# Performance work log

Measured on AMD Instinct MI355X. Metric: run time of the kernel, lower is better.

The kernel has to match this reference:

```python
import jax, jax.numpy as jnp
import numpy as np

IN_FEATURE = 256
OUT_FEATURE = 128
ALPHA = 0.5  # LeakyReLU negative slope
NEG_BIG = -9e15


def setup_inputs() -> dict:
    key = jax.random.key(0)
    k1, k2, k3, k4 = jax.random.split(key, 4)
    N = 8192
    x = jax.random.normal(k1, (N, IN_FEATURE), dtype=jnp.float32)
    adj = jax.random.randint(k2, (N, N), 0, 2, dtype=jnp.int32)
    stdv = 1.0 / np.sqrt(OUT_FEATURE)
    W = jax.random.uniform(k3, (IN_FEATURE, OUT_FEATURE), dtype=jnp.float32,
                           minval=-stdv, maxval=stdv)
    a = jax.random.uniform(k4, (2 * OUT_FEATURE, 1), dtype=jnp.float32,
                           minval=-stdv, maxval=stdv)
    return {"input": x, "adj": adj, "W": W, "a": a}


def reference(input, adj, W, a):
    # h: [N, F_out]
    h = input @ W
    # Additive attention: cat([h_i, h_j]) @ a == h_i @ a1 + h_j @ a2
    a1 = a[:OUT_FEATURE, 0]   # [F_out]
    a2 = a[OUT_FEATURE:, 0]   # [F_out]
    f1 = h @ a1               # [N]  (row / source contribution)
    f2 = h @ a2               # [N]  (col / target contribution)
    e = jax.nn.leaky_relu(f1[:, None] + f2[None, :], negative_slope=ALPHA)  # [N, N]
    scores = jnp.where(adj > 0, e, NEG_BIG)
    attention = jax.nn.softmax(scores, axis=1)  # [N, N]
    h_prime = attention @ h                     # [N, F_out]
    return jax.nn.elu(h_prime)
```

## Files before the change

kernel.cpp:

```cpp
#include <hip/hip_runtime.h>

#define N_NODES 8192
#define IN_F 256
#define OUT_F 128
#define ALPHA 0.5f
#define JC 8
#define KCHUNK 1024
#define ROUNDS 4
#define RSTEPS 8

using short8 = __attribute__((ext_vector_type(8))) short;
using f32x4  = __attribute__((ext_vector_type(4))) float;

__device__ __forceinline__ unsigned short f2bf(float f){
  unsigned int u = __float_as_uint(f);
  u += 0x7fffu + ((u >> 16) & 1u);
  return (unsigned short)(u >> 16);
}

__global__ __launch_bounds__(256) void k_h(const float* __restrict__ x,
                                           const float* __restrict__ W,
                                           float* __restrict__ h){
  __shared__ float xs[16*IN_F];
  const int tid = threadIdx.x;
  const int r0 = blockIdx.x * 16;
  const float4* xg = (const float4*)(x + (size_t)r0*IN_F);
  float4* xl = (float4*)xs;
  #pragma unroll
  for(int i=0;i<4;i++) xl[tid + i*256] = xg[tid + i*256];
  __syncthreads();
  const int wave = tid >> 6, lane = tid & 63;
  float2 acc[4];
  #pragma unroll
  for(int j=0;j<4;j++){ acc[j].x = 0.f; acc[j].y = 0.f; }
  const float2* Wp = (const float2*)W;
  for(int k4=0;k4<IN_F;k4+=4){
    float4 xq[4];
    #pragma unroll
    for(int j=0;j<4;j++) xq[j] = *(const float4*)&xs[(wave*4+j)*IN_F + k4];
    #pragma unroll
    for(int kk=0;kk<4;kk++){
      float2 wv = Wp[(size_t)(k4+kk)*64 + lane];
      #pragma unroll
      for(int j=0;j<4;j++){
        float xv = kk==0?xq[j].x : kk==1?xq[j].y : kk==2?xq[j].z : xq[j].w;
        acc[j].x += xv*wv.x; acc[j].y += xv*wv.y;
      }
    }
  }
  #pragma unroll
  for(int j=0;j<4;j++)
    *(float2*)(h + (size_t)(r0 + wave*4 + j)*OUT_F + lane*2) = acc[j];
}

__global__ __launch_bounds__(256) void k_f(const float* __restrict__ h,
                                           const float* __restrict__ a,
                                           float* __restrict__ f1,
                                           float* __restrict__ f2){
  const int wave = threadIdx.x >> 6, lane = threadIdx.x & 63;
  const int row = blockIdx.x*4 + wave;
  float2 hv = ((const float2*)(h + (size_t)row*OUT_F))[lane];
  float2 a1 = ((const float2*)a)[lane];
  float2 a2 = ((const float2*)(a + OUT_F))[lane];
  float s1 = hv.x*a1.x + hv.y*a1.y;
  float s2 = hv.x*a2.x + hv.y*a2.y;
  #pragma unroll
  for(int off=32; off; off>>=1){
    s1 += __shfl_down(s1, off);
    s2 += __shfl_down(s2, off);
  }
  if(lane == 0){ f1[row] = s1; f2[row] = s2; }
}

#define LDW 132
__global__ __launch_bounds__(256) void k_pack(const float* __restrict__ h,
                                              unsigned short* __restrict__ P){
  __shared__ float ld[32*LDW];
  const int tid = threadIdx.x;
  const int kb = blockIdx.x, j0 = kb*32;
  #pragma unroll
  for(int i=0;i<4;i++){
    int idx = tid + i*256;
    int row = idx >> 5, c4 = (idx & 31)*4;
    *(float4*)&ld[row*LDW + c4] = *(const float4*)(h + (size_t)(j0+row)*OUT_F + c4);
  }
  __syncthreads();
  #pragma unroll
  for(int i=0;i<2;i++){
    int o = tid*2 + i;
    int c = o >> 6, lane = o & 63;
    int q = lane >> 4, n = lane & 15;
    short8 v;
    #pragma unroll
    for(int t=0;t<8;t++) v[t] = (short)f2bf(ld[(q*8+t)*LDW + c*16 + n]);
    *(short8*)(P + ((size_t)(kb*8 + c)*64 + lane)*8) = v;
  }
}

__global__ __launch_bounds__(256, 2) void k_attn(const int* __restrict__ adj,
    const unsigned short* __restrict__ P,
    const float* __restrict__ f1, const float* __restrict__ f2,
    float* __restrict__ part, float* __restrict__ denp){
  __shared__ __align__(16) short Blds[32768];
  const int tid = threadIdx.x;
  const int wave = tid >> 6, lane = tid & 63;
  const int m = lane & 15, q = lane >> 4;
  const int jc = blockIdx.x;
  const int rb = blockIdx.y;
  const int r0w = rb*128 + wave*32;
  const int kb0 = jc * (KCHUNK/32);
  const float rf1a = f1[r0w + m];
  const float rf1b = f1[r0w + 16 + m];
  const int* ap0 = adj + (size_t)(r0w + m)*N_NODES + jc*KCHUNK + q*8;
  const int* ap1 = ap0 + (size_t)16*N_NODES;
  const float* f2p = f2 + jc*KCHUNK + q*8;
  const short8* Pv = (const short8*)P;

  f32x4 acc0[8], acc1[8];
  #pragma unroll
  for(int c=0;c<8;c++){ acc0[c] = (f32x4){0,0,0,0}; acc1[c] = (f32x4){0,0,0,0}; }
  float den0 = 0.f, den1 = 0.f;

  int4 A00 = *(const int4*)(ap0);
  int4 A01 = *(const int4*)(ap0 + 4);
  int4 A10 = *(const int4*)(ap1);
  int4 A11 = *(const int4*)(ap1 + 4);

  auto welem8 = [&](const int4& a, const int4& b, const float4& fa,
                    const float4& fb, float rf1, float& den) -> short8 {
    short8 af; float tv, ev, w;
    #define WE(slot, av, fv)                               \
      tv = rf1 + (fv);                                     \
      ev = tv > 0.f ? tv : ALPHA*tv;                       \
      w  = __expf(ev);                                     \
      w  = ((av) > 0) ? w : 0.f;                           \
      den += w;                                            \
      af[slot] = (short)f2bf(w);
    WE(0,a.x,fa.x) WE(1,a.y,fa.y) WE(2,a.z,fa.z) WE(3,a.w,fa.w)
    WE(4,b.x,fb.x) WE(5,b.y,fb.y) WE(6,b.z,fb.z) WE(7,b.w,fb.w)
    #undef WE
    return af;
  };

  for(int rd=0; rd<ROUNDS; rd++){
    const short8* Ps = Pv + (size_t)(kb0 + rd*8) * 512;
    short8* Bl8 = (short8*)Blds;
    #pragma unroll
    for(int i=0;i<16;i++){
      int idx = i*256 + tid;
      Bl8[idx] = Ps[idx];
    }
    __syncthreads();
    for(int s=0; s<RSTEPS; s++){
      const int gs = rd*RSTEPS + s;
      int4 B00=A00, B01=A01, B10=A10, B11=A11;
      if(gs+1 < ROUNDS*RSTEPS){
        B00 = *(const int4*)(ap0 + (gs+1)*32);
        B01 = *(const int4*)(ap0 + (gs+1)*32 + 4);
        B10 = *(const int4*)(ap1 + (gs+1)*32);
        B11 = *(const int4*)(ap1 + (gs+1)*32 + 4);
      }
      float4 fa = *(const float4*)(f2p + gs*32);
      float4 fb = *(const float4*)(f2p + gs*32 + 4);
      short8 af0 = welem8(A00, A01, fa, fb, rf1a, den0);
      short8 af1 = welem8(A10, A11, fa, fb, rf1b, den1);
      const short8* Bl = (const short8*)Blds + (s*512 + lane);
      #pragma unroll
      for(int c=0;c<8;c++){
        short8 Bf = Bl[c*64];
        acc0[c] = __builtin_amdgcn_mfma_f32_16x16x32_bf16(af0, Bf, acc0[c], 0,0,0);
        acc1[c] = __builtin_amdgcn_mfma_f32_16x16x32_bf16(af1, Bf, acc1[c], 0,0,0);
      }
      A00=B00; A01=B01; A10=B10; A11=B11;
    }
    __syncthreads();
  }

  den0 += __shfl_down(den0, 32); den0 += __shfl_down(den0, 16);
  den1 += __shfl_down(den1, 32); den1 += __shfl_down(den1, 16);
  if(lane < 16){
    denp[(size_t)jc*N_NODES + r0w + lane]      = den0;
    denp[(size_t)jc*N_NODES + r0w + 16 + lane] = den1;
  }
  float* pp = part + (size_t)jc*N_NODES*OUT_F;
  #pragma unroll
  for(int c=0;c<8;c++){
    #pragma unroll
    for(int reg=0;reg<4;reg++){
      pp[(size_t)(r0w + q*4 + reg)*OUT_F      + c*16 + m] = acc0[c][reg];
      pp[(size_t)(r0w + 16 + q*4 + reg)*OUT_F + c*16 + m] = acc1[c][reg];
    }
  }
}

__global__ __launch_bounds__(256) void k_out(const float* __restrict__ part,
    const float* __restrict__ denp, float* __restrict__ out){
  const int idx = blockIdx.x*256 + threadIdx.x;
  const int r = idx >> 7;
  float v = 0.f, d = 0.f;
  #pragma unroll
  for(int p=0;p<JC;p++){
    v += part[(size_t)p*N_NODES*OUT_F + idx];
    d += denp[(size_t)p*N_NODES + r];
  }
  v /= d;
  out[idx] = v > 0.f ? v : (__expf(v) - 1.f);
}

extern "C" void kernel_launch(void* const* d_in, const int* in_sizes, int n_in,
                              void* d_out, int out_size, void* d_ws, size_t ws_size,
                              hipStream_t stream){
  const float* x   = (const float*)d_in[0];
  const int*   adj = (const int*)d_in[1];
  const float* W   = (const float*)d_in[2];
  const float* a   = (const float*)d_in[3];
  char* ws = (char*)d_ws;
  float* h            = (float*)ws;
  unsigned short* P   = (unsigned short*)(ws + (4u<<20));
  float* f1           = (float*)(ws + (6u<<20));
  float* f2           = (float*)(ws + (6u<<20) + (32u<<10));
  float* part         = (float*)(ws + (8u<<20));
  float* denp         = (float*)(ws + (40u<<20));
  float* out          = (float*)d_out;

  k_h<<<512, 256, 0, stream>>>(x, W, h);
  k_f<<<2048, 256, 0, stream>>>(h, a, f1, f2);
  k_pack<<<256, 256, 0, stream>>>(h, P);
  k_attn<<<dim3(JC,64), 256, 0, stream>>>(adj, P, f1, f2, part, denp);
  k_out<<<(N_NODES*OUT_F)/256, 256, 0, stream>>>(part, denp, out);
}
```

Before: 458.3 us.

## Stage attention weights in swizzled LDS with coalesced row-wise adj loads

The attention kernel now has all 256 threads read adj in coalesced row-contiguous int4 chunks, compute the masked exp weights, and write them as bf16 into an XOR-swizzled LDS tile. Each wave then reads its MFMA A fragments from that tile. Previously each lane loaded strided 32-byte pieces of different adj rows straight into registers. The denominator is now summed from the bf16-rounded weights rather than the fp32 values, which changes rounding slightly. The change adds LDS traffic, an extra barrier per round, and doubles the number of rounds, so overlap of adj loads with MFMA work drops.

Measured after the change: 410.3 us. 10.5% less time.

```diff
diff --git a/kernel.cpp b/kernel.cpp
--- a/kernel.cpp
+++ b/kernel.cpp
@@ -6,16 +6,20 @@
 #define ALPHA 0.5f
 #define JC 8
 #define KCHUNK 1024
-#define ROUNDS 4
-#define RSTEPS 8
+#define RK 128
+#define ROUNDS 8
+#define RSTEPS 4
 
 using short8 = __attribute__((ext_vector_type(8))) short;
 using f32x4  = __attribute__((ext_vector_type(4))) float;
 
-__device__ __forceinline__ unsigned short f2bf(float f){
+__device__ __forceinline__ unsigned int f2bf(float f){
   unsigned int u = __float_as_uint(f);
   u += 0x7fffu + ((u >> 16) & 1u);
-  return (unsigned short)(u >> 16);
+  return u >> 16;
+}
+__device__ __forceinline__ float bf2f(short s){
+  return __uint_as_float(((unsigned int)(unsigned short)s) << 16);
 }
 
 __global__ __launch_bounds__(256) void k_h(const float* __restrict__ x,
@@ -101,83 +105,80 @@
     const unsigned short* __restrict__ P,
     const float* __restrict__ f1, const float* __restrict__ f2,
     float* __restrict__ part, float* __restrict__ denp){
-  __shared__ __align__(16) short Blds[32768];
+  __shared__ __align__(16) unsigned short Alds[128*RK];
+  __shared__ __align__(16) short Blds[RK*OUT_F];
+  __shared__ float f1s[128];
   const int tid = threadIdx.x;
   const int wave = tid >> 6, lane = tid & 63;
   const int m = lane & 15, q = lane >> 4;
   const int jc = blockIdx.x;
-  const int rb = blockIdx.y;
-  const int r0w = rb*128 + wave*32;
+  const int r0b = blockIdx.y * 128;
+  const int jb = jc * KCHUNK;
   const int kb0 = jc * (KCHUNK/32);
-  const float rf1a = f1[r0w + m];
-  const float rf1b = f1[r0w + 16 + m];
-  const int* ap0 = adj + (size_t)(r0w + m)*N_NODES + jc*KCHUNK + q*8;
-  const int* ap1 = ap0 + (size_t)16*N_NODES;
-  const float* f2p = f2 + jc*KCHUNK + q*8;
-  const short8* Pv = (const short8*)P;
+  const int srow = tid >> 5;
+  const int sc0  = (tid & 31) * 4;
+  const int swz  = ((((sc0 >> 3) ^ srow) << 4) | ((sc0 & 4) << 1));
+
+  if(tid < 128) f1s[tid] = f1[r0b + tid];
 
   f32x4 acc0[8], acc1[8];
   #pragma unroll
   for(int c=0;c<8;c++){ acc0[c] = (f32x4){0,0,0,0}; acc1[c] = (f32x4){0,0,0,0}; }
   float den0 = 0.f, den1 = 0.f;
 
-  int4 A00 = *(const int4*)(ap0);
-  int4 A01 = *(const int4*)(ap0 + 4);
-  int4 A10 = *(const int4*)(ap1);
-  int4 A11 = *(const int4*)(ap1 + 4);
-
-  auto welem8 = [&](const int4& a, const int4& b, const float4& fa,
-                    const float4& fb, float rf1, float& den) -> short8 {
-    short8 af; float tv, ev, w;
-    #define WE(slot, av, fv)                               \
-      tv = rf1 + (fv);                                     \
-      ev = tv > 0.f ? tv : ALPHA*tv;                       \
-      w  = __expf(ev);                                     \
-      w  = ((av) > 0) ? w : 0.f;                           \
-      den += w;                                            \
-      af[slot] = (short)f2bf(w);
-    WE(0,a.x,fa.x) WE(1,a.y,fa.y) WE(2,a.z,fa.z) WE(3,a.w,fa.w)
-    WE(4,b.x,fb.x) WE(5,b.y,fb.y) WE(6,b.z,fb.z) WE(7,b.w,fb.w)
-    #undef WE
-    return af;
-  };
+  const char* Ab = (const char*)Alds;
+  char* Aw = (char*)Alds + swz;
+  const int mw = m & 7;
+  const int rg0 = wave*32 + m;
+
+  __syncthreads();
 
   for(int rd=0; rd<ROUNDS; rd++){
-    const short8* Ps = Pv + (size_t)(kb0 + rd*8) * 512;
-    short8* Bl8 = (short8*)Blds;
-    #pragma unroll
+    const int kbase = jb + rd*RK;
+    const int4* Pb = (const int4*)(P + ((size_t)(kb0 + rd*4) << 12));
+    int4* Bl4 = (int4*)Blds;
+    #pragma unroll
+    for(int i=0;i<8;i++) Bl4[i*256 + tid] = Pb[i*256 + tid];
+    float4 fv = *(const float4*)(f2 + kbase + sc0);
+    const char* ap = (const char*)adj + (((size_t)(r0b + srow)*N_NODES + kbase + sc0) << 2);
+    #pragma unroll 4
     for(int i=0;i<16;i++){
-      int idx = i*256 + tid;
-      Bl8[idx] = Ps[idx];
+      int4 av = *(const int4*)(ap + ((size_t)i*8*N_NODES << 2));
+      float f1v = f1s[i*8 + srow];
+      float t0 = f1v + fv.x, t1 = f1v + fv.y, t2 = f1v + fv.z, t3 = f1v + fv.w;
+      t0 = t0 > 0.f ? t0 : ALPHA*t0;  t1 = t1 > 0.f ? t1 : ALPHA*t1;
+      t2 = t2 > 0.f ? t2 : ALPHA*t2;  t3 = t3 > 0.f ? t3 : ALPHA*t3;
+      float w0 = av.x > 0 ? __expf(t0) : 0.f;
+      float w1 = av.y > 0 ? __expf(t1) : 0.f;
+      float w2 = av.z > 0 ? __expf(t2) : 0.f;
+      float w3 = av.w > 0 ? __expf(t3) : 0.f;
+      uint2 pk;
+      pk.x = f2bf(w0) | (f2bf(w1) << 16);
+      pk.y = f2bf(w2) | (f2bf(w3) << 16);
+      *(uint2*)(Aw + (i*8 + srow)*(RK*2)) = pk;
     }
     __syncthreads();
-    for(int s=0; s<RSTEPS; s++){
-      const int gs = rd*RSTEPS + s;
-      int4 B00=A00, B01=A01, B10=A10, B11=A11;
-      if(gs+1 < ROUNDS*RSTEPS){
-        B00 = *(const int4*)(ap0 + (gs+1)*32);
-        B01 = *(const int4*)(ap0 + (gs+1)*32 + 4);
-        B10 = *(const int4*)(ap1 + (gs+1)*32);
-        B11 = *(const int4*)(ap1 + (gs+1)*32 + 4);
-      }
-      float4 fa = *(const float4*)(f2p + gs*32);
-      float4 fb = *(const float4*)(f2p + gs*32 + 4);
-      short8 af0 = welem8(A00, A01, fa, fb, rf1a, den0);
-      short8 af1 = welem8(A10, A11, fa, fb, rf1b, den1);
-      const short8* Bl = (const short8*)Blds + (s*512 + lane);
+    #pragma unroll
+    for(int s=0;s<RSTEPS;s++){
+      const int gq = ((s*4 + q) ^ mw) << 4;
+      short8 A0 = *(const short8*)(Ab + rg0*(RK*2) + gq);
+      short8 A1 = *(const short8*)(Ab + (rg0+16)*(RK*2) + gq);
+      #pragma unroll
+      for(int t=0;t<8;t++){ den0 += bf2f(A0[t]); den1 += bf2f(A1[t]); }
+      const short8* Bl = (const short8*)Blds + s*512 + lane;
       #pragma unroll
       for(int c=0;c<8;c++){
         short8 Bf = Bl[c*64];
-        acc0[c] = __builtin_amdgcn_mfma_f32_16x16x32_bf16(af0, Bf, acc0[c], 0,0,0);
-        acc1[c] = __builtin_amdgcn_mfma_f32_16x16x32_bf16(af1, Bf, acc1[c], 0,0,0);
+        acc0[c] = __builtin_amdgcn_mfma_f32_16x16x32_bf16(A0, Bf, acc0[c], 0,0,0);
+        acc1[c] = __builtin_amdgcn_mfma_f32_16x16x32_bf16(A1, Bf, acc1[c], 0,0,0);
       }
-      A00=B00; A01=B01; A10=B10; A11=B11;
     }
     __syncthreads();
   }
 
   den0 += __shfl_down(den0, 32); den0 += __shfl_down(den0, 16);
   den1 += __shfl_down(den1, 32); den1 += __shfl_down(den1, 16);
+  const int r0w = r0b + wave*32;
   if(lane < 16){
     denp[(size_t)jc*N_NODES + r0w + lane]      = den0;
     denp[(size_t)jc*N_NODES + r0w + 16 + lane] = den1;
```
